# Performance work log

Measured on AMD Instinct MI355X. Metric: run time of the kernel, lower is better.

The kernel has to match this reference:

```python
import jax, jax.numpy as jnp
import numpy as np

EMBED = 2048
D_COMPR = 512
D_ROPE = 128
N_HEADS = 8
HEAD_DIM = D_COMPR // N_HEADS  # 64
B, S = 4, 2048


def _lin(x, w, b):
    # torch Linear: y = x @ w.T + b, w: [out, in]
    return jnp.einsum('bsi,oi->bso', x, w) + b


def _rope_emb(seq_len):
    inv_freq = 1.0 / (10000.0 ** (jnp.arange(0, D_ROPE, 2, dtype=jnp.float32) / D_ROPE))
    t = jnp.arange(seq_len, dtype=jnp.float32)
    freqs = jnp.einsum('i,j->ij', t, inv_freq)           # [S, D_ROPE/2]
    return jnp.concatenate([freqs, freqs], axis=-1)      # [S, D_ROPE]


def _apply_rope(x, emb):
    # x: [B, S, D_ROPE], emb: [S, D_ROPE]
    cos, sin = jnp.cos(emb), jnp.sin(emb)
    x1, x2 = jnp.split(x, 2, axis=-1)
    rot = jnp.concatenate([-x2, x1], axis=-1)
    return x * cos + rot * sin


def setup_inputs() -> dict:
    key = jax.random.key(0)
    ks = jax.random.split(key, 20)
    sc = 0.02
    inp = {'x': jax.random.normal(ks[0], (B, S, EMBED), dtype=jnp.float32)}
    def w(k, o, i):
        return jax.random.normal(k, (o, i), dtype=jnp.float32) * sc
    inp['CQ_w'] = w(ks[1], D_COMPR, EMBED); inp['CQ_b'] = jnp.zeros((D_COMPR,), jnp.float32)
    inp['CQC_w'] = w(ks[2], D_COMPR - D_ROPE, D_COMPR); inp['CQC_b'] = jnp.zeros((D_COMPR - D_ROPE,), jnp.float32)
    inp['CQR_w'] = w(ks[3], D_ROPE, EMBED); inp['CQR_b'] = jnp.zeros((D_ROPE,), jnp.float32)
    inp['CKV_w'] = w(ks[4], D_COMPR, EMBED); inp['CKV_b'] = jnp.zeros((D_COMPR,), jnp.float32)
    inp['CKR_w'] = w(ks[5], D_ROPE, EMBED); inp['CKR_b'] = jnp.zeros((D_ROPE,), jnp.float32)
    inp['CKC_w'] = w(ks[6], D_COMPR - D_ROPE, D_COMPR); inp['CKC_b'] = jnp.zeros((D_COMPR - D_ROPE,), jnp.float32)
    inp['CV_w'] = w(ks[7], D_COMPR, D_COMPR); inp['CV_b'] = jnp.zeros((D_COMPR,), jnp.float32)
    inp['OUT_w'] = w(ks[8], EMBED, D_COMPR); inp['OUT_b'] = jnp.zeros((EMBED,), jnp.float32)
    return inp


def reference(x, CQ_w, CQ_b, CQC_w, CQC_b, CQR_w, CQR_b, CKV_w, CKV_b,
              CKR_w, CKR_b, CKC_w, CKC_b, CV_w, CV_b, OUT_w, OUT_b):
    b, s, _ = x.shape
    gelu = lambda t: jax.nn.gelu(t, approximate=False)

    cq = gelu(_lin(x, CQ_w, CQ_b))                # [B,S,D_COMPR]
    cqc = _lin(cq, CQC_w, CQC_b)                  # [B,S,D_COMPR-D_ROPE]
    cqr = _lin(x, CQR_w, CQR_b)                   # [B,S,D_ROPE]
    ckv = gelu(_lin(x, CKV_w, CKV_b))             # [B,S,D_COMPR]
    ckr = _lin(x, CKR_w, CKR_b)                   # [B,S,D_ROPE]
    ckc = _lin(ckv, CKC_w, CKC_b)                 # [B,S,D_COMPR-D_ROPE]

    emb = _rope_emb(s)
    cqr = _apply_rope(cqr, emb)
    ckr = _apply_rope(ckr, emb)

    Q = gelu(jnp.concatenate([cqc, cqr], axis=-1))  # [B,S,D_COMPR]
    K = gelu(jnp.concatenate([ckc, ckr], axis=-1))
    V = _lin(ckv, CV_w, CV_b)

    Q = Q.reshape(b, s, N_HEADS, HEAD_DIM).transpose(0, 2, 1, 3)  # [B,H,S,D]
    K = K.reshape(b, s, N_HEADS, HEAD_DIM).transpose(0, 2, 1, 3)
    V = V.reshape(b, s, N_HEADS, HEAD_DIM).transpose(0, 2, 1, 3)

    scale = 1.0 / np.sqrt(HEAD_DIM).astype(np.float32)
    scores = jnp.einsum('bhqd,bhkd->bhqk', Q, K) * scale
    causal = jnp.triu(jnp.ones((s, s), dtype=bool), k=1)
    scores = jnp.where(causal[None, None], -jnp.inf, scores)
    attn = jax.nn.softmax(scores, axis=-1)
    out = jnp.einsum('bhqk,bhkd->bhqd', attn, V)
    out = out.transpose(0, 2, 1, 3).reshape(b, s, D_COMPR)
    return _lin(out, OUT_w, OUT_b)
```

## Files before the change

kernel.cpp:

```cpp
#include <hip/hip_runtime.h>
#include <cstdint>
#include <cstddef>

typedef unsigned short u16;
typedef short bf16x8 __attribute__((ext_vector_type(8)));
typedef float f32x4 __attribute__((ext_vector_type(4)));
typedef unsigned short u16x8 __attribute__((ext_vector_type(8)));

#define DEVINL __device__ __forceinline__

DEVINL u16 f2bf(float f) {
  union { float f; unsigned u; } v; v.f = f;
  unsigned r = v.u + 0x7FFFu + ((v.u >> 16) & 1u);
  return (u16)(r >> 16);
}
DEVINL float bf2f(u16 h) {
  union { unsigned u; float f; } v; v.u = ((unsigned)h) << 16;
  return v.f;
}
DEVINL float gelu_exact(float x) {
  return 0.5f * x * (1.0f + erff(x * 0.70710678118654752f));
}
DEVINL void gload_lds16(const void* g, void* l) {
  __builtin_amdgcn_global_load_lds(
      (const __attribute__((address_space(1))) void*)g,
      (__attribute__((address_space(3))) void*)l, 16, 0, 0);
}
DEVINL bf16x8 ld_frag(const u16* p) {
  return *reinterpret_cast<const bf16x8*>(p);
}

__global__ __launch_bounds__(256) void conv_f32_bf16(
    const float* __restrict__ src, u16* __restrict__ dst, int n4) {
  int i = blockIdx.x * 256 + threadIdx.x;
  int stride = gridDim.x * 256;
  for (; i < n4; i += stride) {
    float4 v = reinterpret_cast<const float4*>(src)[i];
    ushort4 o;
    o.x = f2bf(v.x); o.y = f2bf(v.y); o.z = f2bf(v.z); o.w = f2bf(v.w);
    reinterpret_cast<ushort4*>(dst)[i] = o;
  }
}

struct ConvTab {
  const float* src[8];
  u16* dst[8];
  int bstart[8];
};
__global__ __launch_bounds__(256) void conv_w_fused(ConvTab t) {
  int blk = blockIdx.x;
  int seg = 0;
#pragma unroll
  for (int i = 1; i < 8; ++i)
    if (blk >= t.bstart[i]) seg = i;
  const float* src = t.src[seg];
  u16* dst = t.dst[seg];
  int base = (blk - t.bstart[seg]) * 1024 + threadIdx.x;
#pragma unroll
  for (int k = 0; k < 4; ++k) {
    int i = base + k * 256;
    float4 v = reinterpret_cast<const float4*>(src)[i];
    ushort4 o;
    o.x = f2bf(v.x); o.y = f2bf(v.y); o.z = f2bf(v.z); o.w = f2bf(v.w);
    reinterpret_cast<ushort4*>(dst)[i] = o;
  }
}

struct EpiSeg {
  const float* bias;
  void* dst;
  int stride;
  int col_start;
  int do_gelu;
};
struct EpiTable { EpiSeg s[4]; int nseg; };

template <int F32OUT>
__global__ __launch_bounds__(256) void gemm_bt(
    const u16* __restrict__ A, const u16* __restrict__ W, int K, EpiTable et) {
  __shared__ u16 As[128 * 32];
  __shared__ u16 Bs[128 * 32];
  const int tid = threadIdx.x;
  const int lane = tid & 63;
  const int wv = tid >> 6;
  const int g = lane >> 4;
  const int c = lane & 15;
  const int wr = (wv >> 1) * 64;
  const int wc = (wv & 1) * 64;

  int bx = blockIdx.x, by = blockIdx.y;
  {
    int nwg = gridDim.x * gridDim.y;
    if ((nwg & 7) == 0) {
      int lid = by * gridDim.x + bx;
      int qq = nwg >> 3;
      int swz = (lid & 7) * qq + (lid >> 3);
      bx = swz % gridDim.x;
      by = swz / gridDim.x;
    }
  }
  const long long rowBase = (long long)bx * 128;
  const long long colBase = (long long)by * 128;

  f32x4 acc[4][4];
#pragma unroll
  for (int m = 0; m < 4; ++m)
#pragma unroll
    for (int n = 0; n < 4; ++n) acc[m][n] = {0.f, 0.f, 0.f, 0.f};

  const int r0 = tid >> 2, sp0 = tid & 3;
  const int scol = (sp0 ^ ((r0 >> 1) & 3)) * 8;
  const u16* Ag = A + (rowBase + r0) * K + scol;
  const u16* Wg = W + (colBase + r0) * K + scol;
  u16* Al0 = As + tid * 8;
  u16* Al1 = As + (256 + tid) * 8;
  u16* Bl0 = Bs + tid * 8;
  u16* Bl1 = Bs + (256 + tid) * 8;
  const long long skip = 64LL * K;

  int aoff[4], boff[4];
#pragma unroll
  for (int m = 0; m < 4; ++m) {
    int row = wr + m * 16 + c;
    aoff[m] = row * 32 + ((g ^ ((row >> 1) & 3)) * 8);
    int rowb = wc + m * 16 + c;
    boff[m] = rowb * 32 + ((g ^ ((rowb >> 1) & 3)) * 8);
  }

  const int nk = K >> 5;
  for (int kt = 0; kt < nk; ++kt) {
    const int k0 = kt * 32;
    gload_lds16(Ag + k0, Al0);
    gload_lds16(Ag + skip + k0, Al1);
    gload_lds16(Wg + k0, Bl0);
    gload_lds16(Wg + skip + k0, Bl1);
    __syncthreads();
    bf16x8 a[4], b[4];
#pragma unroll
    for (int m = 0; m < 4; ++m) a[m] = ld_frag(&As[aoff[m]]);
#pragma unroll
    for (int n = 0; n < 4; ++n) b[n] = ld_frag(&Bs[boff[n]]);
#pragma unroll
    for (int m = 0; m < 4; ++m)
#pragma unroll
      for (int n = 0; n < 4; ++n)
        acc[m][n] = __builtin_amdgcn_mfma_f32_16x16x32_bf16(a[m], b[n], acc[m][n], 0, 0, 0);
    __syncthreads();
  }

  EpiSeg e = et.s[0];
#pragma unroll
  for (int i = 1; i < 4; ++i)
    if (i < et.nseg && (int)colBase >= et.s[i].col_start) e = et.s[i];

#pragma unroll
  for (int m = 0; m < 4; ++m) {
#pragma unroll
    for (int n = 0; n < 4; ++n) {
      int col = (int)colBase + wc + n * 16 + c;
      int dcol = col - e.col_start;
      float bias = e.bias[dcol];
#pragma unroll
      for (int r = 0; r < 4; ++r) {
        long long row = rowBase + wr + m * 16 + g * 4 + r;
        float v = acc[m][n][r] + bias;
        if (e.do_gelu) v = gelu_exact(v);
        if (F32OUT)
          ((float*)e.dst)[row * e.stride + dcol] = v;
        else
          ((u16*)e.dst)[row * e.stride + dcol] = f2bf(v);
      }
    }
  }
}

__global__ __launch_bounds__(256) void rope_gelu_k(
    const u16* __restrict__ cqr, const u16* __restrict__ ckr,
    u16* __restrict__ Qb, u16* __restrict__ Kb) {
  int idx = blockIdx.x * 256 + threadIdx.x;
  int row = idx >> 6, j = idx & 63;
  int s = row & 2047;
  float invf = exp2f(-(float)j * (13.287712379549449f / 64.f));
  float th = (float)s * invf;
  float sn, cs;
  sincosf(th, &sn, &cs);
  long long r128 = (long long)row * 128;
  float q1 = bf2f(cqr[r128 + j]), q2 = bf2f(cqr[r128 + 64 + j]);
  float k1 = bf2f(ckr[r128 + j]), k2 = bf2f(ckr[r128 + 64 + j]);
  float qo1 = q1 * cs - q2 * sn, qo2 = q2 * cs + q1 * sn;
  float ko1 = k1 * cs - k2 * sn, ko2 = k2 * cs + k1 * sn;
  long long rb = (long long)row * 512;
  Qb[rb + 384 + j] = f2bf(gelu_exact(qo1));
  Qb[rb + 448 + j] = f2bf(gelu_exact(qo2));
  Kb[rb + 384 + j] = f2bf(gelu_exact(ko1));
  Kb[rb + 448 + j] = f2bf(gelu_exact(ko2));
}

__global__ __launch_bounds__(256) void attn_fwd(
    const u16* __restrict__ Q, const u16* __restrict__ Kin,
    const u16* __restrict__ V, u16* __restrict__ O) {
  const int p = blockIdx.x;
  const int bh = blockIdx.y;
  const int b = bh >> 3, h = bh & 7;
  const int tid = threadIdx.x, lane = tid & 63, wv = tid >> 6;
  const int g = lane >> 4, c = lane & 15;

  __shared__ u16 Ks[64 * 64];
  __shared__ u16 Vt[64 * 72];
  __shared__ u16 Ps[2][64 * 72];

  const long long rowB = (long long)b * 2048;
  const int qb[2] = { p * 64, (31 - p) * 64 };
  const u16* Kp = Kin + rowB * 512 + h * 64;
  const u16* Vp = V + rowB * 512 + h * 64;

  bf16x8 qa[2][2];
#pragma unroll
  for (int tl = 0; tl < 2; ++tl) {
    const u16* Qp = Q + (rowB + qb[tl] + wv * 16 + c) * 512 + h * 64;
#pragma unroll
    for (int kc = 0; kc < 2; ++kc)
      qa[tl][kc] = ld_frag(Qp + kc * 32 + g * 8);
  }

  f32x4 o[2][4];
  float m_[2][4], l_[2][4];
#pragma unroll
  for (int tl = 0; tl < 2; ++tl) {
#pragma unroll
    for (int nf = 0; nf < 4; ++nf) o[tl][nf] = {0.f, 0.f, 0.f, 0.f};
#pragma unroll
    for (int r = 0; r < 4; ++r) { m_[tl][r] = -1e30f; l_[tl][r] = 0.f; }
  }

  const int kr0 = tid >> 3, ksp = tid & 7;
  const int ksrc = (ksp ^ (kr0 & 7)) * 8;
  const int vkv0 = tid >> 3, vd0 = (tid & 7) * 8;
  const float SCL2 = 0.18033688011112042f;

  const int nt = 32 - p;
  for (int t = 0; t < nt; ++t) {
    const int kvb = t * 64;
    const bool doA = (t <= p);
    gload_lds16(Kp + (long long)(kvb + kr0) * 512 + ksrc, Ks + tid * 8);
    gload_lds16(Kp + (long long)(kvb + kr0 + 32) * 512 + ksrc, Ks + (256 + tid) * 8);
    u16x8 v0 = *reinterpret_cast<const u16x8*>(Vp + (long long)(kvb + vkv0) * 512 + vd0);
    u16x8 v1 = *reinterpret_cast<const u16x8*>(Vp + (long long)(kvb + vkv0 + 32) * 512 + vd0);
    __syncthreads();
#pragma unroll
    for (int i = 0; i < 8; ++i) {
      Vt[(vd0 + i) * 72 + vkv0] = v0[i];
      Vt[(vd0 + i) * 72 + vkv0 + 32] = v1[i];
    }
    __syncthreads();

    f32x4 s[2][4];
#pragma unroll
    for (int tl = 0; tl < 2; ++tl)
#pragma unroll
      for (int nf = 0; nf < 4; ++nf) s[tl][nf] = {0.f, 0.f, 0.f, 0.f};
#pragma unroll
    for (int kc = 0; kc < 2; ++kc) {
      bf16x8 kb[4];
#pragma unroll
      for (int nf = 0; nf < 4; ++nf) {
        int kvr = nf * 16 + c;
        int slot = (kc * 4 + g) ^ (kvr & 7);
        kb[nf] = ld_frag(&Ks[kvr * 64 + slot * 8]);
      }
#pragma unroll
      for (int nf = 0; nf < 4; ++nf)
        s[1][nf] = __builtin_amdgcn_mfma_f32_16x16x32_bf16(qa[1][kc], kb[nf], s[1][nf], 0, 0, 0);
      if (doA) {
#pragma unroll
        for (int nf = 0; nf < 4; ++nf)
          s[0][nf] = __builtin_amdgcn_mfma_f32_16x16x32_bf16(qa[0][kc], kb[nf], s[0][nf], 0, 0, 0);
      }
    }

#pragma unroll
    for (int tl = 0; tl < 2; ++tl) {
      if (tl == 0 && !doA) continue;
      const bool diag = (tl == 0) ? (t == p) : (t == nt - 1);
      const int qr0 = qb[tl] + wv * 16 + g * 4;
#pragma unroll
      for (int r = 0; r < 4; ++r) {
        float vmax = -1e30f;
#pragma unroll
        for (int nf = 0; nf < 4; ++nf) {
          float sv = s[tl][nf][r] * SCL2;
          if (diag && (kvb + nf * 16 + c > qr0 + r)) sv = -1e30f;
          s[tl][nf][r] = sv;
          vmax = fmaxf(vmax, sv);
        }
#pragma unroll
        for (int sh = 1; sh < 16; sh <<= 1)
          vmax = fmaxf(vmax, __shfl_xor(vmax, sh, 64));
        float mo = m_[tl][r];
        float mn = fmaxf(mo, vmax);
        float corr = exp2f(mo - mn);
        float ps = 0.f;
#pragma unroll
        for (int nf = 0; nf < 4; ++nf) {
          float pv = exp2f(s[tl][nf][r] - mn);
          s[tl][nf][r] = pv;
          ps += pv;
        }
#pragma unroll
        for (int sh = 1; sh < 16; sh <<= 1)
          ps += __shfl_xor(ps, sh, 64);
        m_[tl][r] = mn;
        l_[tl][r] = l_[tl][r] * corr + ps;
#pragma unroll
        for (int nf = 0; nf < 4; ++nf) o[tl][nf][r] *= corr;
      }
#pragma unroll
      for (int nf = 0; nf < 4; ++nf)
#pragma unroll
        for (int r = 0; r < 4; ++r)
          Ps[tl][(wv * 16 + g * 4 + r) * 72 + nf * 16 + c] = f2bf(s[tl][nf][r]);
    }
    __syncthreads();

#pragma unroll
    for (int kc2 = 0; kc2 < 2; ++kc2) {
      bf16x8 vb[4];
#pragma unroll
      for (int nf = 0; nf < 4; ++nf)
        vb[nf] = ld_frag(&Vt[(nf * 16 + c) * 72 + kc2 * 32 + g * 8]);
      bf16x8 pb = ld_frag(&Ps[1][(wv * 16 + c) * 72 + kc2 * 32 + g * 8]);
#pragma unroll
      for (int nf = 0; nf < 4; ++nf)
        o[1][nf] = __builtin_amdgcn_mfma_f32_16x16x32_bf16(pb, vb[nf], o[1][nf], 0, 0, 0);
      if (doA) {
        bf16x8 pa = ld_frag(&Ps[0][(wv * 16 + c) * 72 + kc2 * 32 + g * 8]);
#pragma unroll
        for (int nf = 0; nf < 4; ++nf)
          o[0][nf] = __builtin_amdgcn_mfma_f32_16x16x32_bf16(pa, vb[nf], o[0][nf], 0, 0, 0);
      }
    }
  }

#pragma unroll
  for (int tl = 0; tl < 2; ++tl) {
#pragma unroll
    for (int r = 0; r < 4; ++r) {
      float inv = 1.0f / l_[tl][r];
      long long row = rowB + qb[tl] + wv * 16 + g * 4 + r;
#pragma unroll
      for (int nf = 0; nf < 4; ++nf)
        O[row * 512 + h * 64 + nf * 16 + c] = f2bf(o[tl][nf][r] * inv);
    }
  }
}

extern "C" void kernel_launch(void* const* d_in, const int* in_sizes, int n_in,
                              void* d_out, int out_size, void* d_ws, size_t ws_size,
                              hipStream_t stream) {
  const float* x = (const float*)d_in[0];
  const float* CQ_w = (const float*)d_in[1];   const float* CQ_b = (const float*)d_in[2];
  const float* CQC_w = (const float*)d_in[3];  const float* CQC_b = (const float*)d_in[4];
  const float* CQR_w = (const float*)d_in[5];  const float* CQR_b = (const float*)d_in[6];
  const float* CKV_w = (const float*)d_in[7];  const float* CKV_b = (const float*)d_in[8];
  const float* CKR_w = (const float*)d_in[9];  const float* CKR_b = (const float*)d_in[10];
  const float* CKC_w = (const float*)d_in[11]; const float* CKC_b = (const float*)d_in[12];
  const float* CV_w = (const float*)d_in[13];  const float* CV_b = (const float*)d_in[14];
  const float* OUT_w = (const float*)d_in[15]; const float* OUT_b = (const float*)d_in[16];
  float* out = (float*)d_out;

  char* ws = (char*)d_ws;
  size_t off = 0;
  auto alloc = [&](size_t bytes) -> void* {
    void* pp = ws + off;
    off += (bytes + 255) & ~(size_t)255;
    return pp;
  };
  u16* xb   = (u16*)alloc(8192ULL * 2048 * 2);
  u16* Wc1  = (u16*)alloc(1280ULL * 2048 * 2);
  u16* Wcqc = (u16*)alloc(384ULL * 512 * 2);
  u16* Wc2  = (u16*)alloc(896ULL * 512 * 2);
  u16* Wout = (u16*)alloc(2048ULL * 512 * 2);
  u16* cq   = (u16*)alloc(8192ULL * 512 * 2);
  u16* ckv  = (u16*)alloc(8192ULL * 512 * 2);
  u16* cqrt = (u16*)alloc(8192ULL * 128 * 2);
  u16* ckrt = (u16*)alloc(8192ULL * 128 * 2);
  u16* Qb   = (u16*)alloc(8192ULL * 512 * 2);
  u16* Kbf  = (u16*)alloc(8192ULL * 512 * 2);
  u16* Vb   = (u16*)alloc(8192ULL * 512 * 2);
  u16* AO   = (u16*)alloc(8192ULL * 512 * 2);
  (void)ws_size; (void)in_sizes; (void)n_in; (void)out_size;

  conv_f32_bf16<<<2048, 256, 0, stream>>>(x, xb, 8192 * 2048 / 4);

  ConvTab ct;
  ct.src[0] = CQ_w;  ct.dst[0] = Wc1;
  ct.src[1] = CKV_w; ct.dst[1] = Wc1 + 512 * 2048;
  ct.src[2] = CQR_w; ct.dst[2] = Wc1 + 1024 * 2048;
  ct.src[3] = CKR_w; ct.dst[3] = Wc1 + 1152 * 2048;
  ct.src[4] = CQC_w; ct.dst[4] = Wcqc;
  ct.src[5] = CKC_w; ct.dst[5] = Wc2;
  ct.src[6] = CV_w;  ct.dst[6] = Wc2 + 384 * 512;
  ct.src[7] = OUT_w; ct.dst[7] = Wout;
  int bs = 0;
  int nblk[8] = {256, 256, 64, 64, 48, 48, 64, 256};
  for (int i = 0; i < 8; ++i) { ct.bstart[i] = bs; bs += nblk[i]; }
  conv_w_fused<<<bs, 256, 0, stream>>>(ct);

  EpiTable t1 = {};
  t1.nseg = 4;
  t1.s[0] = { CQ_b,  cq,   512, 0,    1 };
  t1.s[1] = { CKV_b, ckv,  512, 512,  1 };
  t1.s[2] = { CQR_b, cqrt, 128, 1024, 0 };
  t1.s[3] = { CKR_b, ckrt, 128, 1152, 0 };
  gemm_bt<0><<<dim3(64, 10), 256, 0, stream>>>(xb, Wc1, 2048, t1);

  rope_gelu_k<<<dim3(8192 * 64 / 256), 256, 0, stream>>>(cqrt, ckrt, Qb, Kbf);

  EpiTable t2 = {};
  t2.nseg = 1;
  t2.s[0] = { CQC_b, Qb, 512, 0, 1 };
  gemm_bt<0><<<dim3(64, 3), 256, 0, stream>>>(cq, Wcqc, 512, t2);

  EpiTable t3 = {};
  t3.nseg = 2;
  t3.s[0] = { CKC_b, Kbf, 512, 0, 1 };
  t3.s[1] = { CV_b,  Vb,  512, 384, 0 };
  gemm_bt<0><<<dim3(64, 7), 256, 0, stream>>>(ckv, Wc2, 512, t3);

  attn_fwd<<<dim3(16, 32), 256, 0, stream>>>(Qb, Kbf, Vb, AO);

  EpiTable t4 = {};
  t4.nseg = 1;
  t4.s[0] = { OUT_b, out, 2048, 0, 0 };
  gemm_bt<1><<<dim3(64, 16), 256, 0, stream>>>(AO, Wout, 512, t4);
}
```

Before: 447.7 us.

## Widen attention KV tile to 128 and skip unneeded softmax rescales

The attention loop now processes 128 keys per iteration instead of 64. This halves the iteration count and the number of barriers, and each staged K/V tile feeds more MFMA work. The double P buffer becomes one wave-private buffer, and the PV product is done per query tile right after its softmax. The running-max correction is applied only when the row max actually increases. In exchange, LDS use per block grows, which can lower occupancy, and register pressure rises from the doubled score fragments.

New measurement: 499.2 us. 11.5% more time.

```diff
diff --git a/kernel.cpp b/kernel.cpp
--- a/kernel.cpp
+++ b/kernel.cpp
@@ -205,9 +205,9 @@
   const int tid = threadIdx.x, lane = tid & 63, wv = tid >> 6;
   const int g = lane >> 4, c = lane & 15;
 
-  __shared__ u16 Ks[64 * 64];
-  __shared__ u16 Vt[64 * 72];
-  __shared__ u16 Ps[2][64 * 72];
+  __shared__ u16 Ks[128 * 64];
+  __shared__ u16 Vt[64 * 136];
+  __shared__ u16 Ps[64 * 136];
 
   const long long rowB = (long long)b * 2048;
   const int qb[2] = { p * 64, (31 - p) * 64 };
@@ -233,61 +233,68 @@
     for (int r = 0; r < 4; ++r) { m_[tl][r] = -1e30f; l_[tl][r] = 0.f; }
   }
 
-  const int kr0 = tid >> 3, ksp = tid & 7;
-  const int ksrc = (ksp ^ (kr0 & 7)) * 8;
+  const int srow = tid >> 3, ssp = tid & 7;
+  const int ksrc = (ssp ^ (srow & 7)) * 8;
   const int vkv0 = tid >> 3, vd0 = (tid & 7) * 8;
   const float SCL2 = 0.18033688011112042f;
 
-  const int nt = 32 - p;
+  const int lastA = p >> 1;
+  const int nt = ((31 - p) >> 1) + 1;
   for (int t = 0; t < nt; ++t) {
-    const int kvb = t * 64;
-    const bool doA = (t <= p);
-    gload_lds16(Kp + (long long)(kvb + kr0) * 512 + ksrc, Ks + tid * 8);
-    gload_lds16(Kp + (long long)(kvb + kr0 + 32) * 512 + ksrc, Ks + (256 + tid) * 8);
-    u16x8 v0 = *reinterpret_cast<const u16x8*>(Vp + (long long)(kvb + vkv0) * 512 + vd0);
-    u16x8 v1 = *reinterpret_cast<const u16x8*>(Vp + (long long)(kvb + vkv0 + 32) * 512 + vd0);
+    const int kvb = t * 128;
+    const bool doA = (t <= lastA);
+#pragma unroll
+    for (int it = 0; it < 4; ++it)
+      gload_lds16(Kp + (long long)(kvb + it * 32 + srow) * 512 + ksrc,
+                  Ks + (it * 256 + tid) * 8);
+    u16x8 vr[4];
+#pragma unroll
+    for (int j = 0; j < 4; ++j)
+      vr[j] = *reinterpret_cast<const u16x8*>(
+          Vp + (long long)(kvb + vkv0 + j * 32) * 512 + vd0);
     __syncthreads();
 #pragma unroll
-    for (int i = 0; i < 8; ++i) {
-      Vt[(vd0 + i) * 72 + vkv0] = v0[i];
-      Vt[(vd0 + i) * 72 + vkv0 + 32] = v1[i];
-    }
+    for (int j = 0; j < 4; ++j)
+#pragma unroll
+      for (int i = 0; i < 8; ++i)
+        Vt[(vd0 + i) * 136 + vkv0 + j * 32] = vr[j][i];
     __syncthreads();
 
-    f32x4 s[2][4];
+    f32x4 s[2][8];
 #pragma unroll
     for (int tl = 0; tl < 2; ++tl)
 #pragma unroll
-      for (int nf = 0; nf < 4; ++nf) s[tl][nf] = {0.f, 0.f, 0.f, 0.f};
+      for (int nf = 0; nf < 8; ++nf) s[tl][nf] = {0.f, 0.f, 0.f, 0.f};
 #pragma unroll
     for (int kc = 0; kc < 2; ++kc) {
-      bf16x8 kb[4];
-#pragma unroll
-      for (int nf = 0; nf < 4; ++nf) {
+      bf16x8 kb[8];
+#pragma unroll
+      for (int nf = 0; nf < 8; ++nf) {
         int kvr = nf * 16 + c;
         int slot = (kc * 4 + g) ^ (kvr & 7);
         kb[nf] = ld_frag(&Ks[kvr * 64 + slot * 8]);
       }
 #pragma unroll
-      for (int nf = 0; nf < 4; ++nf)
+      for (int nf = 0; nf < 8; ++nf)
         s[1][nf] = __builtin_amdgcn_mfma_f32_16x16x32_bf16(qa[1][kc], kb[nf], s[1][nf], 0, 0, 0);
       if (doA) {
 #pragma unroll
-        for (int nf = 0; nf < 4; ++nf)
+        for (int nf = 0; nf < 8; ++nf)
           s[0][nf] = __builtin_amdgcn_mfma_f32_16x16x32_bf16(qa[0][kc], kb[nf], s[0][nf], 0, 0, 0);
       }
     }
+    __syncthreads();
 
 #pragma unroll
     for (int tl = 0; tl < 2; ++tl) {
       if (tl == 0 && !doA) continue;
-      const bool diag = (tl == 0) ? (t == p) : (t == nt - 1);
+      const bool diag = (tl == 0) ? (t == lastA) : (t == nt - 1);
       const int qr0 = qb[tl] + wv * 16 + g * 4;
 #pragma unroll
       for (int r = 0; r < 4; ++r) {
         float vmax = -1e30f;
 #pragma unroll
-        for (int nf = 0; nf < 4; ++nf) {
+        for (int nf = 0; nf < 8; ++nf) {
           float sv = s[tl][nf][r] * SCL2;
           if (diag && (kvb + nf * 16 + c > qr0 + r)) sv = -1e30f;
           s[tl][nf][r] = sv;
@@ -298,10 +305,9 @@
           vmax = fmaxf(vmax, __shfl_xor(vmax, sh, 64));
         float mo = m_[tl][r];
         float mn = fmaxf(mo, vmax);
-        float corr = exp2f(mo - mn);
         float ps = 0.f;
 #pragma unroll
-        for (int nf = 0; nf < 4; ++nf) {
+        for (int nf = 0; nf < 8; ++nf) {
           float pv = exp2f(s[tl][nf][r] - mn);
           s[tl][nf][r] = pv;
           ps += pv;
@@ -309,34 +315,28 @@
 #pragma unroll
         for (int sh = 1; sh < 16; sh <<= 1)
           ps += __shfl_xor(ps, sh, 64);
-        m_[tl][r] = mn;
-        l_[tl][r] = l_[tl][r] * corr + ps;
-#pragma unroll
-        for (int nf = 0; nf < 4; ++nf) o[tl][nf][r] *= corr;
+        if (mn > mo) {
+          float corr = exp2f(mo - mn);
+          l_[tl][r] = l_[tl][r] * corr;
+#pragma unroll
+          for (int nf = 0; nf < 4; ++nf) o[tl][nf][r] *= corr;
+          m_[tl][r] = mn;
+        }
+        l_[tl][r] += ps;
       }
 #pragma unroll
-      for (int nf = 0; nf < 4; ++nf)
+      for (int nf = 0; nf < 8; ++nf)
 #pragma unroll
         for (int r = 0; r < 4; ++r)
-          Ps[tl][(wv * 16 + g * 4 + r) * 72 + nf * 16 + c] = f2bf(s[tl][nf][r]);
-    }
-    __syncthreads();
-
-#pragma unroll
-    for (int kc2 = 0; kc2 < 2; ++kc2) {
-      bf16x8 vb[4];
-#pragma unroll
-      for (int nf = 0; nf < 4; ++nf)
-        vb[nf] = ld_frag(&Vt[(nf * 16 + c) * 72 + kc2 * 32 + g * 8]);
-      bf16x8 pb = ld_frag(&Ps[1][(wv * 16 + c) * 72 + kc2 * 32 + g * 8]);
-#pragma unroll
-      for (int nf = 0; nf < 4; ++nf)
-        o[1][nf] = __builtin_amdgcn_mfma_f32_16x16x32_bf16(pb, vb[nf], o[1][nf], 0, 0, 0);
-      if (doA) {
-        bf16x8 pa = ld_frag(&Ps[0][(wv * 16 + c) * 72 + kc2 * 32 + g * 8]);
-#pragma unroll
-        for (int nf = 0; nf < 4; ++nf)
-          o[0][nf] = __builtin_amdgcn_mfma_f32_16x16x32_bf16(pa, vb[nf], o[0][nf], 0, 0, 0);
+          Ps[(wv * 16 + g * 4 + r) * 136 + nf * 16 + c] = f2bf(s[tl][nf][r]);
+#pragma unroll
+      for (int kc2 = 0; kc2 < 4; ++kc2) {
+        bf16x8 pa = ld_frag(&Ps[(wv * 16 + c) * 136 + kc2 * 32 + g * 8]);
+#pragma unroll
+        for (int nf = 0; nf < 4; ++nf) {
+          bf16x8 vb = ld_frag(&Vt[(nf * 16 + c) * 136 + kc2 * 32 + g * 8]);
+          o[tl][nf] = __builtin_amdgcn_mfma_f32_16x16x32_bf16(pa, vb, o[tl][nf], 0, 0, 0);
+        }
       }
     }
   }
```

## Split attention into 32-row query tiles with 128-thread blocks and twice the grid

Applied to the files above, without the earlier changes.

The attention kernel now uses 2 waves per block, each block handling two 32-row query tiles paired from opposite ends of the causal triangle, and launches twice as many blocks (32x32). The P buffer in shared memory is merged into a single 64-row buffer shared by both tiles. Each tile's PV product now runs right after its softmax instead of after a block barrier, with a new barrier placed after the QK MFMAs. The goal is more blocks and better load balance across CUs. The cost is that each block loads every K/V tile for only 32 query rows, which roughly doubles global K/V traffic per unit of work.

New measurement: 470.0 us. 1.05x slower.

```diff
diff --git a/kernel.cpp b/kernel.cpp
--- a/kernel.cpp
+++ b/kernel.cpp
@@ -196,7 +196,7 @@
   Kb[rb + 448 + j] = f2bf(gelu_exact(ko2));
 }
 
-__global__ __launch_bounds__(256) void attn_fwd(
+__global__ __launch_bounds__(128) void attn_fwd(
     const u16* __restrict__ Q, const u16* __restrict__ Kin,
     const u16* __restrict__ V, u16* __restrict__ O) {
   const int p = blockIdx.x;
@@ -207,10 +207,10 @@
 
   __shared__ u16 Ks[64 * 64];
   __shared__ u16 Vt[64 * 72];
-  __shared__ u16 Ps[2][64 * 72];
+  __shared__ u16 Ps[64 * 72];
 
   const long long rowB = (long long)b * 2048;
-  const int qb[2] = { p * 64, (31 - p) * 64 };
+  const int qb[2] = { p * 32, (63 - p) * 32 };
   const u16* Kp = Kin + rowB * 512 + h * 64;
   const u16* Vp = V + rowB * 512 + h * 64;
 
@@ -233,25 +233,31 @@
     for (int r = 0; r < 4; ++r) { m_[tl][r] = -1e30f; l_[tl][r] = 0.f; }
   }
 
-  const int kr0 = tid >> 3, ksp = tid & 7;
-  const int ksrc = (ksp ^ (kr0 & 7)) * 8;
+  const int srow = tid >> 3, ssp = tid & 7;
+  const int ksrc = (ssp ^ (srow & 7)) * 8;
   const int vkv0 = tid >> 3, vd0 = (tid & 7) * 8;
   const float SCL2 = 0.18033688011112042f;
 
-  const int nt = 32 - p;
+  const int lastA = p >> 1;
+  const int nt = 32 - (p >> 1);
   for (int t = 0; t < nt; ++t) {
     const int kvb = t * 64;
-    const bool doA = (t <= p);
-    gload_lds16(Kp + (long long)(kvb + kr0) * 512 + ksrc, Ks + tid * 8);
-    gload_lds16(Kp + (long long)(kvb + kr0 + 32) * 512 + ksrc, Ks + (256 + tid) * 8);
-    u16x8 v0 = *reinterpret_cast<const u16x8*>(Vp + (long long)(kvb + vkv0) * 512 + vd0);
-    u16x8 v1 = *reinterpret_cast<const u16x8*>(Vp + (long long)(kvb + vkv0 + 32) * 512 + vd0);
+    const bool doA = (t <= lastA);
+#pragma unroll
+    for (int it = 0; it < 4; ++it)
+      gload_lds16(Kp + (long long)(kvb + it * 16 + srow) * 512 + ksrc,
+                  Ks + (it * 128 + tid) * 8);
+    u16x8 vr[4];
+#pragma unroll
+    for (int j = 0; j < 4; ++j)
+      vr[j] = *reinterpret_cast<const u16x8*>(
+          Vp + (long long)(kvb + vkv0 + j * 16) * 512 + vd0);
     __syncthreads();
 #pragma unroll
-    for (int i = 0; i < 8; ++i) {
-      Vt[(vd0 + i) * 72 + vkv0] = v0[i];
-      Vt[(vd0 + i) * 72 + vkv0 + 32] = v1[i];
-    }
+    for (int j = 0; j < 4; ++j)
+#pragma unroll
+      for (int i = 0; i < 8; ++i)
+        Vt[(vd0 + i) * 72 + vkv0 + j * 16] = vr[j][i];
     __syncthreads();
 
     f32x4 s[2][4];
@@ -277,12 +283,14 @@
           s[0][nf] = __builtin_amdgcn_mfma_f32_16x16x32_bf16(qa[0][kc], kb[nf], s[0][nf], 0, 0, 0);
       }
     }
+    __syncthreads();
 
 #pragma unroll
     for (int tl = 0; tl < 2; ++tl) {
       if (tl == 0 && !doA) continue;
-      const bool diag = (tl == 0) ? (t == p) : (t == nt - 1);
+      const bool diag = (tl == 0) ? (t == lastA) : (t == nt - 1);
       const int qr0 = qb[tl] + wv * 16 + g * 4;
+      const int prow = tl * 32 + wv * 16;
 #pragma unroll
       for (int r = 0; r < 4; ++r) {
         float vmax = -1e30f;
@@ -318,25 +326,15 @@
       for (int nf = 0; nf < 4; ++nf)
 #pragma unroll
         for (int r = 0; r < 4; ++r)
-          Ps[tl][(wv * 16 + g * 4 + r) * 72 + nf * 16 + c] = f2bf(s[tl][nf][r]);
-    }
-    __syncthreads();
-
-#pragma unroll
-    for (int kc2 = 0; kc2 < 2; ++kc2) {
-      bf16x8 vb[4];
-#pragma unroll
-      for (int nf = 0; nf < 4; ++nf)
-        vb[nf] = ld_frag(&Vt[(nf * 16 + c) * 72 + kc2 * 32 + g * 8]);
-      bf16x8 pb = ld_frag(&Ps[1][(wv * 16 + c) * 72 + kc2 * 32 + g * 8]);
-#pragma unroll
-      for (int nf = 0; nf < 4; ++nf)
-        o[1][nf] = __builtin_amdgcn_mfma_f32_16x16x32_bf16(pb, vb[nf], o[1][nf], 0, 0, 0);
-      if (doA) {
-        bf16x8 pa = ld_frag(&Ps[0][(wv * 16 + c) * 72 + kc2 * 32 + g * 8]);
-#pragma unroll
-        for (int nf = 0; nf < 4; ++nf)
-          o[0][nf] = __builtin_amdgcn_mfma_f32_16x16x32_bf16(pa, vb[nf], o[0][nf], 0, 0, 0);
+          Ps[(prow + g * 4 + r) * 72 + nf * 16 + c] = f2bf(s[tl][nf][r]);
+#pragma unroll
+      for (int kc2 = 0; kc2 < 2; ++kc2) {
+        bf16x8 pa = ld_frag(&Ps[(prow + c) * 72 + kc2 * 32 + g * 8]);
+#pragma unroll
+        for (int nf = 0; nf < 4; ++nf) {
+          bf16x8 vb = ld_frag(&Vt[(nf * 16 + c) * 72 + kc2 * 32 + g * 8]);
+          o[tl][nf] = __builtin_amdgcn_mfma_f32_16x16x32_bf16(pa, vb, o[tl][nf], 0, 0, 0);
+        }
       }
     }
   }
@@ -427,7 +425,7 @@
   t3.s[1] = { CV_b,  Vb,  512, 384, 0 };
   gemm_bt<0><<<dim3(64, 7), 256, 0, stream>>>(ckv, Wc2, 512, t3);
 
-  attn_fwd<<<dim3(16, 32), 256, 0, stream>>>(Qb, Kbf, Vb, AO);
+  attn_fwd<<<dim3(32, 32), 128, 0, stream>>>(Qb, Kbf, Vb, AO);
 
   EpiTable t4 = {};
   t4.nseg = 1;
```
